# Optimization experiments

Measured on AMD Instinct MI355X. Metric: run time of the kernel, lower is better.

## Reference

```python
import jax, jax.numpy as jnp
import numpy as np

B, CIN, COUT, K, H, W, NPTS = 8, 256, 256, 4, 128, 128, 512


def setup_inputs() -> dict:
    key = jax.random.key(0)
    ks = jax.random.split(key, 9)
    inp = {
        'input': jax.random.normal(ks[0], (B, CIN, H, W), dtype=jnp.float32),
        'ax': jax.random.uniform(ks[1], (B, NPTS), dtype=jnp.float32) * (W - 1),
        'ay': jax.random.uniform(ks[2], (B, NPTS), dtype=jnp.float32) * (H - 1),
        # 1x1 conv = matmul over channels
        'Wp': jax.random.normal(ks[3], (COUT, CIN), dtype=jnp.float32) * 0.02,
        'bp': jnp.zeros((COUT,), dtype=jnp.float32),
        'Woff': jax.random.normal(ks[4], (K, 2, CIN), dtype=jnp.float32) * 0.02,
        'boff': jnp.zeros((K, 2), dtype=jnp.float32),
        'Ww': jax.random.normal(ks[5], (K, CIN), dtype=jnp.float32) * 0.02,
        'bw': jnp.zeros((K,), dtype=jnp.float32),
    }
    return inp


def _bilinear_zeros(img, xs, ys):
    """grid_sample(mode='bilinear', padding_mode='zeros').
    img: [b, C, H, W]; xs, ys: [b, H, W] source pixel coords. Returns [b, H, W, C]."""
    b, C, h, w = img.shape
    img_hwc = jnp.transpose(img, (0, 2, 3, 1))  # [b, H, W, C]
    x0 = jnp.floor(xs)
    y0 = jnp.floor(ys)
    wx1 = xs - x0
    wy1 = ys - y0
    bidx = jnp.arange(b)[:, None, None]

    def corner(xi, yi, wgt):
        valid = (xi >= 0) & (xi < w) & (yi >= 0) & (yi < h)
        xc = jnp.clip(xi, 0, w - 1).astype(jnp.int32)
        yc = jnp.clip(yi, 0, h - 1).astype(jnp.int32)
        v = img_hwc[bidx, yc, xc]  # [b, H, W, C]
        return v * (jnp.where(valid, wgt, 0.0))[..., None]

    out = (corner(x0, y0, (1 - wx1) * (1 - wy1))
           + corner(x0 + 1, y0, wx1 * (1 - wy1))
           + corner(x0, y0 + 1, (1 - wx1) * wy1)
           + corner(x0 + 1, y0 + 1, wx1 * wy1))
    return out


def _forward(input, ax, ay, Wp, bp, Woff, boff, Ww, bw):
    b, c, h, w = input.shape
    k = Ww.shape[0]
    proj = jnp.einsum('bchw,oc->bohw', input, Wp) + bp[None, :, None, None]
    # k flow fields [k, b, 2, h, w]
    flows = jnp.einsum('bchw,koc->kbohw', input, Woff) + boff[:, None, :, None, None]
    logits = jnp.einsum('bchw,kc->bkhw', input, Ww) + bw[None, :, None, None]
    wts = jax.nn.softmax(logits, axis=1)  # [b, k, h, w]

    gx = jnp.arange(w, dtype=input.dtype)[None, None, :]
    gy = jnp.arange(h, dtype=input.dtype)[None, :, None]
    # torch normalization: n = 2*v/(dim-1)-1, then grid_sample(align_corners=False)
    # maps n -> ((n+1)*dim - 1)/2 = v*dim/(dim-1) - 0.5
    sx_scale = w / max(w - 1, 1)
    sy_scale = h / max(h - 1, 1)

    # gather sum_k wts_k * sampled_k at every pixel (loop over small fixed k)
    summed = jnp.zeros((b, h, w, proj.shape[1]), dtype=input.dtype)
    for i in range(k):
        sx = (gx + flows[i, :, 0]) * sx_scale - 0.5  # [b, h, w]
        sy = (gy + flows[i, :, 1]) * sy_scale - 0.5
        summed = summed + wts[:, i, :, :, None] * _bilinear_zeros(proj, sx, sy)

    # point gather: feat[num, :, id[1], id[0]] with id = trunc((ax, ay))
    ix = jnp.trunc(ax).astype(jnp.int32)  # width index
    iy = jnp.trunc(ay).astype(jnp.int32)  # height index
    out = summed[jnp.arange(b)[:, None], iy, ix]  # [b, num_pts, out_ch]
    return out


def reference(input, ax, ay, Wp, bp, Woff, boff, Ww, bw):
    return _forward(input, ax, ay, Wp, bp, Woff, boff, Ww, bw)
```

## Files before the change

### kernel.cpp

```cpp
#include <hip/hip_runtime.h>
#include <hip/hip_fp16.h>

#define B_      8
#define CIN_    256
#define COUT_   256
#define K_      4
#define H_      128
#define W_      128
#define NPTS_   512

#define NPTS_TOT_   (B_ * NPTS_)
#define T_BYTES_    ((size_t)B_ * H_ * W_ * CIN_ * sizeof(__half))
#define WTS_OFF_    T_BYTES_
#define SITES_OFF_  (WTS_OFF_   + (size_t)NPTS_TOT_ * 16 * 4)
#define WSUM_OFF_   (SITES_OFF_ + (size_t)NPTS_TOT_ * 16 * 4)
#define WS_NEED_    (WSUM_OFF_  + (size_t)NPTS_TOT_ * 4)

typedef __attribute__((ext_vector_type(8))) short short8v;
typedef __attribute__((ext_vector_type(4))) float f32x4;

__device__ __forceinline__ unsigned int bf16pair(float a, float b) {
    unsigned int ua = __float_as_uint(a), ub = __float_as_uint(b);
    ua = (ua + 0x7FFFu + ((ua >> 16) & 1u)) >> 16;
    ub = (ub + 0x7FFFu + ((ub >> 16) & 1u)) >> 16;
    return ua | (ub << 16);
}

__global__ __launch_bounds__(256) void ka_kernel(
    const float* __restrict__ input,
    const float* __restrict__ ax,
    const float* __restrict__ ay,
    const float* __restrict__ Woff,
    const float* __restrict__ boff,
    const float* __restrict__ Ww,
    const float* __restrict__ bw,
    __half* __restrict__ T,
    float* __restrict__ wts_g,
    int*   __restrict__ sites_g,
    float* __restrict__ wsums_g)
{
    __shared__ float lt[32][129];
    __shared__ float xs[CIN_];
    __shared__ float dotv[12];
    __shared__ float wc16[16];

    const int bid = blockIdx.x;
    const int t   = threadIdx.x;

    if (bid < 8192) {
        const int b   = bid >> 10;
        const int r   = bid & 1023;
        const int h   = r >> 3;
        const int c0  = (r & 7) << 5;

        const int c = t >> 3;
        const int m = t & 7;
        const float* __restrict__ src = input + (((size_t)(b * CIN_ + c0 + c) * H_ + h) * W_);
        #pragma unroll
        for (int q = 0; q < 4; ++q) {
            const int w = m * 4 + q * 32;
            const float4 v = *reinterpret_cast<const float4*>(src + w);
            lt[c][w]     = v.x;
            lt[c][w + 1] = v.y;
            lt[c][w + 2] = v.z;
            lt[c][w + 3] = v.w;
        }
        __syncthreads();

        const int wph = t >> 2;
        const int j0  = (t & 3) << 3;
        #pragma unroll
        for (int g = 0; g < 2; ++g) {
            const int w = wph + (g << 6);
            unsigned int words[4];
            #pragma unroll
            for (int i = 0; i < 4; ++i) {
                __half2 h2 = __floats2half2_rn(lt[j0 + 2 * i][w], lt[j0 + 2 * i + 1][w]);
                words[i] = *reinterpret_cast<unsigned int*>(&h2);
            }
            __half* dst = T + (((size_t)(b * H_ + h) * W_ + w) * CIN_ + c0 + j0);
            *reinterpret_cast<uint4*>(dst) = make_uint4(words[0], words[1], words[2], words[3]);
        }
        return;
    }

    const int pt = bid - 8192;
    const int b  = pt >> 9;

    const int ix = (int)truncf(ax[pt]);
    const int iy = (int)truncf(ay[pt]);
    const float* __restrict__ chan = input + (size_t)b * (CIN_ * H_ * W_) + (size_t)t * (H_ * W_);

    xs[t] = chan[iy * W_ + ix];
    __syncthreads();

    const int wave = t >> 6;
    const int lane = t & 63;
    #pragma unroll
    for (int r = 0; r < 3; ++r) {
        const int d = wave * 3 + r;
        const float* __restrict__ row = (d < 8) ? (Woff + d * CIN_) : (Ww + (d - 8) * CIN_);
        float s = 0.f;
        #pragma unroll
        for (int q = 0; q < 4; ++q) {
            const int c = lane + q * 64;
            s = fmaf(xs[c], row[c], s);
        }
        #pragma unroll
        for (int off = 32; off > 0; off >>= 1)
            s += __shfl_down(s, off);
        if (lane == 0) dotv[d] = s;
    }
    __syncthreads();

    if (t < 4) {
        const int k = t;
        const float l0 = dotv[8]  + bw[0];
        const float l1 = dotv[9]  + bw[1];
        const float l2 = dotv[10] + bw[2];
        const float l3 = dotv[11] + bw[3];
        const float mx = fmaxf(fmaxf(l0, l1), fmaxf(l2, l3));
        const float e0 = expf(l0 - mx), e1 = expf(l1 - mx);
        const float e2 = expf(l2 - mx), e3 = expf(l3 - mx);
        const float ek = (k == 0) ? e0 : (k == 1) ? e1 : (k == 2) ? e2 : e3;
        const float wk = ek / (e0 + e1 + e2 + e3);

        const float scale = 128.0f / 127.0f;
        const float fx = dotv[2 * k]     + boff[2 * k];
        const float fy = dotv[2 * k + 1] + boff[2 * k + 1];
        const float sxv = ((float)ix + fx) * scale - 0.5f;
        const float syv = ((float)iy + fy) * scale - 0.5f;
        const float x0f = floorf(sxv), y0f = floorf(syv);
        const float wx1 = sxv - x0f, wy1 = syv - y0f;
        const int x0 = (int)x0f, y0 = (int)y0f;
        #pragma unroll
        for (int ci = 0; ci < 4; ++ci) {
            const int xi = x0 + (ci & 1);
            const int yi = y0 + (ci >> 1);
            const bool valid = (xi >= 0) & (xi < W_) & (yi >= 0) & (yi < H_);
            float wc = ((ci & 1) ? wx1 : 1.f - wx1) * ((ci >> 1) ? wy1 : 1.f - wy1) * wk;
            wc = valid ? wc : 0.f;
            const int xc = min(max(xi, 0), W_ - 1);
            const int yc = min(max(yi, 0), H_ - 1);
            const int idx = k * 4 + ci;
            wc16[idx] = wc;
            wts_g[pt * 16 + idx]   = wc;
            sites_g[pt * 16 + idx] = ((b * H_ + yc) * W_ + xc) * CIN_;
        }
    }
    __syncthreads();
    if (t == 0) {
        float s = 0.f;
        #pragma unroll
        for (int i = 0; i < 16; ++i) s += wc16[i];
        wsums_g[pt] = s;
    }
}

__global__ __launch_bounds__(512) void kb_kernel(
    const __half* __restrict__ T,
    const float* __restrict__ Wp,
    const float* __restrict__ bp,
    const float* __restrict__ wts_g,
    const int*   __restrict__ sites_g,
    const float* __restrict__ wsums_g,
    float* __restrict__ out)
{
    __shared__ float xsh[16][268];
    __shared__ unsigned short wb[128 * 40];
    __shared__ float swts[16][16];
    __shared__ int   ssites[16][16];
    __shared__ float swsum[16];

    const int blk = blockIdx.x;
    const int pg  = blk >> 1;
    const int nh  = blk & 1;
    const int p0g = pg << 4;
    const int tid = threadIdx.x;

    if (tid < 256) {
        swts[tid >> 4][tid & 15]   = wts_g[p0g * 16 + tid];
        ssites[tid >> 4][tid & 15] = sites_g[p0g * 16 + tid];
    } else if (tid < 256 + 16) {
        swsum[tid - 256] = wsums_g[p0g + (tid - 256)];
    }
    __syncthreads();

    {
        const int p   = tid >> 5;
        const int oct = tid & 31;
        const int c0  = oct << 3;
        float a[8] = {0.f, 0.f, 0.f, 0.f, 0.f, 0.f, 0.f, 0.f};
        #pragma unroll
        for (int s = 0; s < 16; ++s) {
            const float w = swts[p][s];
            const uint4 raw = *reinterpret_cast<const uint4*>(T + (size_t)ssites[p][s] + c0);
            const __half* hv = reinterpret_cast<const __half*>(&raw);
            #pragma unroll
            for (int j = 0; j < 8; ++j)
                a[j] = fmaf(w, __half2float(hv[j]), a[j]);
        }
        *reinterpret_cast<float4*>(&xsh[p][c0])     = make_float4(a[0], a[1], a[2], a[3]);
        *reinterpret_cast<float4*>(&xsh[p][c0 + 4]) = make_float4(a[4], a[5], a[6], a[7]);
    }
    __syncthreads();

    const int wave = tid >> 6;
    const int lane = tid & 63;
    const int mn   = lane & 15;
    const int kb4  = lane >> 4;
    const int n0   = nh * 128 + wave * 16;

    const float bpv = bp[n0 + mn];
    f32x4 acc;
    acc[0] = bpv * swsum[kb4 * 4 + 0];
    acc[1] = bpv * swsum[kb4 * 4 + 1];
    acc[2] = bpv * swsum[kb4 * 4 + 2];
    acc[3] = bpv * swsum[kb4 * 4 + 3];

    for (int ch = 0; ch < 8; ++ch) {
        #pragma unroll
        for (int r = 0; r < 2; ++r) {
            const int idx = r * 512 + tid;
            const int o   = idx >> 3;
            const int q   = idx & 7;
            const float4 v = *reinterpret_cast<const float4*>(
                Wp + (size_t)(nh * 128 + o) * CIN_ + ch * 32 + q * 4);
            unsigned int* w32 = reinterpret_cast<unsigned int*>(&wb[o * 40 + q * 4]);
            w32[0] = bf16pair(v.x, v.y);
            w32[1] = bf16pair(v.z, v.w);
        }
        __syncthreads();

        const float* xrow = &xsh[mn][ch * 32 + kb4 * 8];
        const float4 xa = *reinterpret_cast<const float4*>(xrow);
        const float4 xb = *reinterpret_cast<const float4*>(xrow + 4);
        union { unsigned int u[4]; short8v v; } af;
        af.u[0] = bf16pair(xa.x, xa.y);
        af.u[1] = bf16pair(xa.z, xa.w);
        af.u[2] = bf16pair(xb.x, xb.y);
        af.u[3] = bf16pair(xb.z, xb.w);

        const short8v bf = *reinterpret_cast<const short8v*>(&wb[(wave * 16 + mn) * 40 + kb4 * 8]);

        acc = __builtin_amdgcn_mfma_f32_16x16x32_bf16(af.v, bf, acc, 0, 0, 0);
        __syncthreads();
    }

    #pragma unroll
    for (int j = 0; j < 4; ++j)
        out[(size_t)(p0g + kb4 * 4 + j) * COUT_ + n0 + mn] = acc[j];
}

__global__ __launch_bounds__(256) void ple_point_kernel(
    const float* __restrict__ input, const float* __restrict__ ax,
    const float* __restrict__ ay, const float* __restrict__ Wp,
    const float* __restrict__ bp, const float* __restrict__ Woff,
    const float* __restrict__ boff, const float* __restrict__ Ww,
    const float* __restrict__ bw, float* __restrict__ out)
{
    const int gid = blockIdx.x;
    const int b   = gid >> 9;
    const int tid = threadIdx.x;

    __shared__ float xs[CIN_];
    __shared__ float dotv[12];

    const int ix = (int)truncf(ax[gid]);
    const int iy = (int)truncf(ay[gid]);
    const float* __restrict__ chan = input + (size_t)b * (CIN_ * H_ * W_) + (size_t)tid * (H_ * W_);

    xs[tid] = chan[iy * W_ + ix];
    __syncthreads();

    const int wave = tid >> 6;
    const int lane = tid & 63;
    #pragma unroll
    for (int r = 0; r < 3; ++r) {
        const int d = wave * 3 + r;
        const float* __restrict__ row = (d < 8) ? (Woff + d * CIN_) : (Ww + (d - 8) * CIN_);
        float s = 0.f;
        #pragma unroll
        for (int q = 0; q < 4; ++q) s = fmaf(xs[lane + q * 64], row[lane + q * 64], s);
        #pragma unroll
        for (int off = 32; off > 0; off >>= 1) s += __shfl_down(s, off);
        if (lane == 0) dotv[d] = s;
    }
    __syncthreads();

    float lg[K_];
    float mx = -1e30f;
    #pragma unroll
    for (int k = 0; k < K_; ++k) { lg[k] = dotv[8 + k] + bw[k]; mx = fmaxf(mx, lg[k]); }
    float se = 0.f;
    #pragma unroll
    for (int k = 0; k < K_; ++k) { lg[k] = expf(lg[k] - mx); se += lg[k]; }
    const float inv_se = 1.f / se;
    const float scale = 128.0f / 127.0f;

    float xacc = 0.f, wsum = 0.f;
    #pragma unroll
    for (int k = 0; k < K_; ++k) {
        const float wk = lg[k] * inv_se;
        const float fx = dotv[2 * k] + boff[2 * k];
        const float fy = dotv[2 * k + 1] + boff[2 * k + 1];
        const float sxv = ((float)ix + fx) * scale - 0.5f;
        const float syv = ((float)iy + fy) * scale - 0.5f;
        const float x0f = floorf(sxv), y0f = floorf(syv);
        const float wx1 = sxv - x0f, wy1 = syv - y0f;
        const int x0 = (int)x0f, y0 = (int)y0f;
        const int x1 = x0 + 1, y1 = y0 + 1;
        const float w00 = (1.f - wx1) * (1.f - wy1) * wk;
        const float w10 = wx1 * (1.f - wy1) * wk;
        const float w01 = (1.f - wx1) * wy1 * wk;
        const float w11 = wx1 * wy1 * wk;
        const bool vx0 = (x0 >= 0) && (x0 < W_);
        const bool vx1 = (x1 >= 0) && (x1 < W_);
        if (y0 >= 0 && y0 < H_) {
            const float* rowp = chan + y0 * W_;
            if (vx0) { xacc = fmaf(w00, rowp[x0], xacc); wsum += w00; }
            if (vx1) { xacc = fmaf(w10, rowp[x1], xacc); wsum += w10; }
        }
        if (y1 >= 0 && y1 < H_) {
            const float* rowp = chan + y1 * W_;
            if (vx0) { xacc = fmaf(w01, rowp[x0], xacc); wsum += w01; }
            if (vx1) { xacc = fmaf(w11, rowp[x1], xacc); wsum += w11; }
        }
    }

    xs[tid] = xacc;
    __syncthreads();

    const float* __restrict__ wrow = Wp + tid * CIN_;
    float a0 = bp[tid] * wsum, a1 = 0.f, a2 = 0.f, a3 = 0.f;
    #pragma unroll 4
    for (int c = 0; c < CIN_; c += 4) {
        const float4 wvv = *reinterpret_cast<const float4*>(wrow + c);
        a0 = fmaf(wvv.x, xs[c], a0);
        a1 = fmaf(wvv.y, xs[c + 1], a1);
        a2 = fmaf(wvv.z, xs[c + 2], a2);
        a3 = fmaf(wvv.w, xs[c + 3], a3);
    }
    out[(size_t)gid * COUT_ + tid] = (a0 + a1) + (a2 + a3);
}

extern "C" void kernel_launch(void* const* d_in, const int* in_sizes, int n_in,
                              void* d_out, int out_size, void* d_ws, size_t ws_size,
                              hipStream_t stream) {
    const float* input = (const float*)d_in[0];
    const float* ax    = (const float*)d_in[1];
    const float* ay    = (const float*)d_in[2];
    const float* Wp    = (const float*)d_in[3];
    const float* bp    = (const float*)d_in[4];
    const float* Woff  = (const float*)d_in[5];
    const float* boff  = (const float*)d_in[6];
    const float* Ww    = (const float*)d_in[7];
    const float* bw    = (const float*)d_in[8];
    float* out = (float*)d_out;

    if (ws_size >= WS_NEED_) {
        __half* T       = (__half*)d_ws;
        float*  wts_g   = (float*)((char*)d_ws + WTS_OFF_);
        int*    sites_g = (int*)  ((char*)d_ws + SITES_OFF_);
        float*  wsums_g = (float*)((char*)d_ws + WSUM_OFF_);

        ka_kernel<<<dim3(8192 + NPTS_TOT_), dim3(256), 0, stream>>>(
            input, ax, ay, Woff, boff, Ww, bw, T, wts_g, sites_g, wsums_g);
        kb_kernel<<<dim3(512), dim3(512), 0, stream>>>(
            T, Wp, bp, wts_g, sites_g, wsums_g, out);
    } else {
        ple_point_kernel<<<dim3(B_ * NPTS_), dim3(256), 0, stream>>>(
            input, ax, ay, Wp, bp, Woff, boff, Ww, bw, out);
    }
}
```

Measured before the change: 66.54 us.

## Apply projection GEMM to full image before gathering sampled points

The channel projection is moved ahead of the bilinear gather: the first kernel now runs a bf16 MFMA GEMM over every pixel, writing projected features in fp16 HWC layout. The second kernel only gathers and weights 16 sites per point, and the weight-sum bias trick is dropped. This removes the separate per-point GEMM and the transposed-input intermediate. In exchange it does far more matrix work, since every pixel is projected, and each block re-reads and converts the full weight matrix.

```diff
diff --git a/kernel.cpp b/kernel.cpp
--- a/kernel.cpp
+++ b/kernel.cpp
@@ -8,13 +8,15 @@
 #define H_      128
 #define W_      128
 #define NPTS_   512
+#define HW_     (H_ * W_)
 
 #define NPTS_TOT_   (B_ * NPTS_)
-#define T_BYTES_    ((size_t)B_ * H_ * W_ * CIN_ * sizeof(__half))
-#define WTS_OFF_    T_BYTES_
+#define PROJ_BYTES_ ((size_t)B_ * HW_ * COUT_ * sizeof(__half))
+#define WTS_OFF_    PROJ_BYTES_
 #define SITES_OFF_  (WTS_OFF_   + (size_t)NPTS_TOT_ * 16 * 4)
-#define WSUM_OFF_   (SITES_OFF_ + (size_t)NPTS_TOT_ * 16 * 4)
-#define WS_NEED_    (WSUM_OFF_  + (size_t)NPTS_TOT_ * 4)
+#define WS_NEED_    (SITES_OFF_ + (size_t)NPTS_TOT_ * 16 * 4)
+
+#define NBLK_GEMM_  ((B_ * HW_) / 64)
 
 typedef __attribute__((ext_vector_type(8))) short short8v;
 typedef __attribute__((ext_vector_type(4))) float f32x4;
@@ -26,70 +28,147 @@
     return ua | (ub << 16);
 }
 
+union GemmSmem {
+    struct {
+        float          lt[32][65];
+        unsigned short A[64 * 40];
+        unsigned short wb[256 * 40];
+    } s;
+    unsigned short ebuf[64][264];
+};
+
 __global__ __launch_bounds__(256) void ka_kernel(
     const float* __restrict__ input,
     const float* __restrict__ ax,
     const float* __restrict__ ay,
+    const float* __restrict__ Wp,
+    const float* __restrict__ bp,
     const float* __restrict__ Woff,
     const float* __restrict__ boff,
     const float* __restrict__ Ww,
     const float* __restrict__ bw,
-    __half* __restrict__ T,
+    __half* __restrict__ proj,
     float* __restrict__ wts_g,
-    int*   __restrict__ sites_g,
-    float* __restrict__ wsums_g)
+    int*   __restrict__ sites_g)
 {
-    __shared__ float lt[32][129];
+    __shared__ GemmSmem sm;
     __shared__ float xs[CIN_];
     __shared__ float dotv[12];
-    __shared__ float wc16[16];
 
     const int bid = blockIdx.x;
     const int t   = threadIdx.x;
 
-    if (bid < 8192) {
-        const int b   = bid >> 10;
-        const int r   = bid & 1023;
-        const int h   = r >> 3;
-        const int c0  = (r & 7) << 5;
-
-        const int c = t >> 3;
-        const int m = t & 7;
-        const float* __restrict__ src = input + (((size_t)(b * CIN_ + c0 + c) * H_ + h) * W_);
-        #pragma unroll
-        for (int q = 0; q < 4; ++q) {
-            const int w = m * 4 + q * 32;
-            const float4 v = *reinterpret_cast<const float4*>(src + w);
-            lt[c][w]     = v.x;
-            lt[c][w + 1] = v.y;
-            lt[c][w + 2] = v.z;
-            lt[c][w + 3] = v.w;
+    if (bid < NBLK_GEMM_) {
+        const int b   = bid >> 8;
+        const int pxl = (bid & 255) << 6;
+        const size_t px0 = (size_t)b * HW_ + pxl;
+
+        const int wave = t >> 6;
+        const int lane = t & 63;
+        const int mn   = lane & 15;
+        const int kb4  = lane >> 4;
+
+        f32x4 acc[4][4];
+        #pragma unroll
+        for (int nf = 0; nf < 4; ++nf) {
+            const float bb = bp[wave * 64 + nf * 16 + mn];
+            #pragma unroll
+            for (int mf = 0; mf < 4; ++mf) {
+                acc[mf][nf][0] = bb; acc[mf][nf][1] = bb;
+                acc[mf][nf][2] = bb; acc[mf][nf][3] = bb;
+            }
+        }
+
+        const int cS = t >> 3;
+        const int mS = t & 7;
+
+        for (int ch = 0; ch < 8; ++ch) {
+            const float* __restrict__ src =
+                input + ((size_t)(b * CIN_ + ch * 32 + cS)) * HW_ + pxl + mS * 4;
+            #pragma unroll
+            for (int q = 0; q < 2; ++q) {
+                const int px = mS * 4 + q * 32;
+                const float4 v = *reinterpret_cast<const float4*>(src + q * 32);
+                sm.s.lt[cS][px]     = v.x;
+                sm.s.lt[cS][px + 1] = v.y;
+                sm.s.lt[cS][px + 2] = v.z;
+                sm.s.lt[cS][px + 3] = v.w;
+            }
+            #pragma unroll
+            for (int r = 0; r < 8; ++r) {
+                const int idx = r * 256 + t;
+                const int o   = idx >> 3;
+                const int q   = idx & 7;
+                const float4 v = *reinterpret_cast<const float4*>(
+                    Wp + (size_t)o * CIN_ + ch * 32 + q * 4);
+                unsigned int* w32 = reinterpret_cast<unsigned int*>(&sm.s.wb[o * 40 + q * 4]);
+                w32[0] = bf16pair(v.x, v.y);
+                w32[1] = bf16pair(v.z, v.w);
+            }
+            __syncthreads();
+
+            {
+                const int px  = t & 63;
+                const int grp = t >> 6;
+                unsigned int u[4];
+                #pragma unroll
+                for (int i = 0; i < 4; ++i)
+                    u[i] = bf16pair(sm.s.lt[grp * 8 + 2 * i][px],
+                                    sm.s.lt[grp * 8 + 2 * i + 1][px]);
+                *reinterpret_cast<uint4*>(&sm.s.A[px * 40 + grp * 8]) =
+                    make_uint4(u[0], u[1], u[2], u[3]);
+            }
+            __syncthreads();
+
+            short8v aF[4];
+            #pragma unroll
+            for (int mf = 0; mf < 4; ++mf)
+                aF[mf] = *reinterpret_cast<const short8v*>(
+                    &sm.s.A[(mf * 16 + mn) * 40 + kb4 * 8]);
+            #pragma unroll
+            for (int nf = 0; nf < 4; ++nf) {
+                const short8v bF = *reinterpret_cast<const short8v*>(
+                    &sm.s.wb[(wave * 64 + nf * 16 + mn) * 40 + kb4 * 8]);
+                #pragma unroll
+                for (int mf = 0; mf < 4; ++mf)
+                    acc[mf][nf] = __builtin_amdgcn_mfma_f32_16x16x32_bf16(
+                        aF[mf], bF, acc[mf][nf], 0, 0, 0);
+            }
+            __syncthreads();
+        }
+
+        #pragma unroll
+        for (int mf = 0; mf < 4; ++mf) {
+            const int row = mf * 16 + kb4 * 4;
+            #pragma unroll
+            for (int nf = 0; nf < 4; ++nf) {
+                const int col = wave * 64 + nf * 16 + mn;
+                #pragma unroll
+                for (int j = 0; j < 4; ++j)
+                    sm.ebuf[row + j][col] = __half_as_ushort(__float2half_rn(acc[mf][nf][j]));
+            }
         }
         __syncthreads();
 
-        const int wph = t >> 2;
-        const int j0  = (t & 3) << 3;
-        #pragma unroll
-        for (int g = 0; g < 2; ++g) {
-            const int w = wph + (g << 6);
-            unsigned int words[4];
-            #pragma unroll
-            for (int i = 0; i < 4; ++i) {
-                __half2 h2 = __floats2half2_rn(lt[j0 + 2 * i][w], lt[j0 + 2 * i + 1][w]);
-                words[i] = *reinterpret_cast<unsigned int*>(&h2);
-            }
-            __half* dst = T + (((size_t)(b * H_ + h) * W_ + w) * CIN_ + c0 + j0);
-            *reinterpret_cast<uint4*>(dst) = make_uint4(words[0], words[1], words[2], words[3]);
+        {
+            const int inner = t & 31;
+            #pragma unroll
+            for (int r = 0; r < 8; ++r) {
+                const int px = (t >> 5) + r * 8;
+                const uint4 v = *reinterpret_cast<const uint4*>(&sm.ebuf[px][inner * 8]);
+                *reinterpret_cast<uint4*>(
+                    reinterpret_cast<unsigned short*>(proj) + (px0 + px) * COUT_ + inner * 8) = v;
+            }
         }
         return;
     }
 
-    const int pt = bid - 8192;
+    const int pt = bid - NBLK_GEMM_;
     const int b  = pt >> 9;
 
     const int ix = (int)truncf(ax[pt]);
     const int iy = (int)truncf(ay[pt]);
-    const float* __restrict__ chan = input + (size_t)b * (CIN_ * H_ * W_) + (size_t)t * (H_ * W_);
+    const float* __restrict__ chan = input + (size_t)b * (CIN_ * HW_) + (size_t)t * HW_;
 
     xs[t] = chan[iy * W_ + ix];
     __syncthreads();
@@ -143,113 +222,49 @@
             const int xc = min(max(xi, 0), W_ - 1);
             const int yc = min(max(yi, 0), H_ - 1);
             const int idx = k * 4 + ci;
-            wc16[idx] = wc;
             wts_g[pt * 16 + idx]   = wc;
-            sites_g[pt * 16 + idx] = ((b * H_ + yc) * W_ + xc) * CIN_;
-        }
-    }
-    __syncthreads();
-    if (t == 0) {
-        float s = 0.f;
-        #pragma unroll
-        for (int i = 0; i < 16; ++i) s += wc16[i];
-        wsums_g[pt] = s;
-    }
-}
-
-__global__ __launch_bounds__(512) void kb_kernel(
-    const __half* __restrict__ T,
-    const float* __restrict__ Wp,
-    const float* __restrict__ bp,
+            sites_g[pt * 16 + idx] = ((b * H_ + yc) * W_ + xc) * COUT_;
+        }
+    }
+}
+
+__global__ __launch_bounds__(512) void kc_kernel(
+    const __half* __restrict__ proj,
     const float* __restrict__ wts_g,
     const int*   __restrict__ sites_g,
-    const float* __restrict__ wsums_g,
     float* __restrict__ out)
 {
-    __shared__ float xsh[16][268];
-    __shared__ unsigned short wb[128 * 40];
     __shared__ float swts[16][16];
     __shared__ int   ssites[16][16];
-    __shared__ float swsum[16];
 
     const int blk = blockIdx.x;
-    const int pg  = blk >> 1;
-    const int nh  = blk & 1;
-    const int p0g = pg << 4;
+    const int p0g = blk << 4;
     const int tid = threadIdx.x;
 
     if (tid < 256) {
         swts[tid >> 4][tid & 15]   = wts_g[p0g * 16 + tid];
         ssites[tid >> 4][tid & 15] = sites_g[p0g * 16 + tid];
-    } else if (tid < 256 + 16) {
-        swsum[tid - 256] = wsums_g[p0g + (tid - 256)];
-    }
-    __syncthreads();
-
-    {
-        const int p   = tid >> 5;
-        const int oct = tid & 31;
-        const int c0  = oct << 3;
-        float a[8] = {0.f, 0.f, 0.f, 0.f, 0.f, 0.f, 0.f, 0.f};
-        #pragma unroll
-        for (int s = 0; s < 16; ++s) {
-            const float w = swts[p][s];
-            const uint4 raw = *reinterpret_cast<const uint4*>(T + (size_t)ssites[p][s] + c0);
-            const __half* hv = reinterpret_cast<const __half*>(&raw);
-            #pragma unroll
-            for (int j = 0; j < 8; ++j)
-                a[j] = fmaf(w, __half2float(hv[j]), a[j]);
-        }
-        *reinterpret_cast<float4*>(&xsh[p][c0])     = make_float4(a[0], a[1], a[2], a[3]);
-        *reinterpret_cast<float4*>(&xsh[p][c0 + 4]) = make_float4(a[4], a[5], a[6], a[7]);
-    }
-    __syncthreads();
-
-    const int wave = tid >> 6;
-    const int lane = tid & 63;
-    const int mn   = lane & 15;
-    const int kb4  = lane >> 4;
-    const int n0   = nh * 128 + wave * 16;
-
-    const float bpv = bp[n0 + mn];
-    f32x4 acc;
-    acc[0] = bpv * swsum[kb4 * 4 + 0];
-    acc[1] = bpv * swsum[kb4 * 4 + 1];
-    acc[2] = bpv * swsum[kb4 * 4 + 2];
-    acc[3] = bpv * swsum[kb4 * 4 + 3];
-
-    for (int ch = 0; ch < 8; ++ch) {
-        #pragma unroll
-        for (int r = 0; r < 2; ++r) {
-            const int idx = r * 512 + tid;
-            const int o   = idx >> 3;
-            const int q   = idx & 7;
-            const float4 v = *reinterpret_cast<const float4*>(
-                Wp + (size_t)(nh * 128 + o) * CIN_ + ch * 32 + q * 4);
-            unsigned int* w32 = reinterpret_cast<unsigned int*>(&wb[o * 40 + q * 4]);
-            w32[0] = bf16pair(v.x, v.y);
-            w32[1] = bf16pair(v.z, v.w);
-        }
-        __syncthreads();
-
-        const float* xrow = &xsh[mn][ch * 32 + kb4 * 8];
-        const float4 xa = *reinterpret_cast<const float4*>(xrow);
-        const float4 xb = *reinterpret_cast<const float4*>(xrow + 4);
-        union { unsigned int u[4]; short8v v; } af;
-        af.u[0] = bf16pair(xa.x, xa.y);
-        af.u[1] = bf16pair(xa.z, xa.w);
-        af.u[2] = bf16pair(xb.x, xb.y);
-        af.u[3] = bf16pair(xb.z, xb.w);
-
-        const short8v bf = *reinterpret_cast<const short8v*>(&wb[(wave * 16 + mn) * 40 + kb4 * 8]);
-
-        acc = __builtin_amdgcn_mfma_f32_16x16x32_bf16(af.v, bf, acc, 0, 0, 0);
-        __syncthreads();
-    }
-
-    #pragma unroll
-    for (int j = 0; j < 4; ++j)
-        out[(size_t)(p0g + kb4 * 4 + j) * COUT_ + n0 + mn] = acc[j];
+    }
+    __syncthreads();
+
+    const int p   = tid >> 5;
+    const int oct = tid & 31;
+    const int c0  = oct << 3;
+
+    float a[8] = {0.f, 0.f, 0.f, 0.f, 0.f, 0.f, 0.f, 0.f};
+    #pragma unroll
+    for (int s = 0; s < 16; ++s) {
+        const float w = swts[p][s];
+        const uint4 raw = *reinterpret_cast<const uint4*>(proj + (size_t)ssites[p][s] + c0);
+        const __half* hv = reinterpret_cast<const __half*>(&raw);
+        #pragma unroll
+        for (int j = 0; j < 8; ++j)
+            a[j] = fmaf(w, __half2float(hv[j]), a[j]);
+    }
+
+    float* orow = out + (size_t)(p0g + p) * COUT_ + c0;
+    *reinterpret_cast<float4*>(orow)     = make_float4(a[0], a[1], a[2], a[3]);
+    *reinterpret_cast<float4*>(orow + 4) = make_float4(a[4], a[5], a[6], a[7]);
 }
 
 __global__ __launch_bounds__(256) void ple_point_kernel(
@@ -268,7 +283,7 @@
 
     const int ix = (int)truncf(ax[gid]);
     const int iy = (int)truncf(ay[gid]);
-    const float* __restrict__ chan = input + (size_t)b * (CIN_ * H_ * W_) + (size_t)tid * (H_ * W_);
+    const float* __restrict__ chan = input + (size_t)b * (CIN_ * HW_) + (size_t)tid * HW_;
 
     xs[tid] = chan[iy * W_ + ix];
     __syncthreads();
@@ -359,15 +374,14 @@
     float* out = (float*)d_out;
 
     if (ws_size >= WS_NEED_) {
-        __half* T       = (__half*)d_ws;
+        __half* proj    = (__half*)d_ws;
         float*  wts_g   = (float*)((char*)d_ws + WTS_OFF_);
         int*    sites_g = (int*)  ((char*)d_ws + SITES_OFF_);
-        float*  wsums_g = (float*)((char*)d_ws + WSUM_OFF_);
-
-        ka_kernel<<<dim3(8192 + NPTS_TOT_), dim3(256), 0, stream>>>(
-            input, ax, ay, Woff, boff, Ww, bw, T, wts_g, sites_g, wsums_g);
-        kb_kernel<<<dim3(512), dim3(512), 0, stream>>>(
-            T, Wp, bp, wts_g, sites_g, wsums_g, out);
+
+        ka_kernel<<<dim3(NBLK_GEMM_ + NPTS_TOT_), dim3(256), 0, stream>>>(
+            input, ax, ay, Wp, bp, Woff, boff, Ww, bw, proj, wts_g, sites_g);
+        kc_kernel<<<dim3(NPTS_TOT_ / 16), dim3(512), 0, stream>>>(
+            proj, wts_g, sites_g, out);
     } else {
         ple_point_kernel<<<dim3(B_ * NPTS_), dim3(256), 0, stream>>>(
             input, ax, ay, Wp, bp, Woff, boff, Ww, bw, out);
```

After: 107.7 us. 61.9% more time.
